# Kernel optimization log

Hardware: AMD Instinct MI355X
Metric: run time of the kernel (lower is better)

Reference implementation:

```python
import jax, jax.numpy as jnp
import numpy as np

NUM_LINKS = 1048576


def _euler_rots(theta):
    # theta: [N,3] -> per-link rotation R = Rz @ Ry @ Rx, shape [N,3,3]
    cx, cy, cz = jnp.cos(theta[:, 0]), jnp.cos(theta[:, 1]), jnp.cos(theta[:, 2])
    sx, sy, sz = jnp.sin(theta[:, 0]), jnp.sin(theta[:, 1]), jnp.sin(theta[:, 2])
    z = jnp.zeros_like(cx)
    o = jnp.ones_like(cx)
    rx = jnp.stack([jnp.stack([o, z, z], -1),
                    jnp.stack([z, cx, -sx], -1),
                    jnp.stack([z, sx, cx], -1)], -2)
    ry = jnp.stack([jnp.stack([cy, z, sy], -1),
                    jnp.stack([z, o, z], -1),
                    jnp.stack([-sy, z, cy], -1)], -2)
    rz = jnp.stack([jnp.stack([cz, -sz, z], -1),
                    jnp.stack([sz, cz, z], -1),
                    jnp.stack([z, z, o], -1)], -2)
    return jnp.matmul(rz, jnp.matmul(ry, rx))  # [N,3,3]


def setup_inputs() -> dict:
    key = jax.random.key(0)
    k1, k2 = jax.random.split(key)
    link_lengths = jax.random.uniform(k1, (NUM_LINKS,), dtype=jnp.float32)
    theta = jax.random.normal(k2, (NUM_LINKS, 3), dtype=jnp.float32)
    return {"link_lengths": link_lengths, "theta": theta}


def reference(link_lengths, theta):
    # Original loop computes eff_pos_i = sum_{j=0..i} (R_0 @ R_1 @ ... @ R_j) @ t_j
    # with t_j = l_j * e_z. Vectorize via prefix matrix products + cumsum.
    R = _euler_rots(theta)                                   # [N,3,3]
    P = jax.lax.associative_scan(jnp.matmul, R)              # P_j = R_0@...@R_j
    v = P[:, :, 2] * link_lengths[:, None]                   # P_j @ (l_j * e_z)
    return jnp.cumsum(v, axis=0)                             # [N,3]
```

## Files before the change

### kernel.cpp

```cpp
#include <hip/hip_runtime.h>
#include <math.h>


#define K1_TPB 512
#define K1_EPT 2
#define K1_EPB (K1_TPB * K1_EPT)
#define K1_NW (K1_TPB / 64)
#define K2_TPB 256
#define K2_EPT 4
#define K2_EPB (K2_TPB * K2_EPT)
#define MAXB 1024
#define EPG (MAXB / K2_TPB)

struct Xf {
    float m[9];
    float p[3];
};

__device__ __forceinline__ void xf_identity(Xf& x) {
    x.m[0] = 1.f; x.m[1] = 0.f; x.m[2] = 0.f;
    x.m[3] = 0.f; x.m[4] = 1.f; x.m[5] = 0.f;
    x.m[6] = 0.f; x.m[7] = 0.f; x.m[8] = 1.f;
    x.p[0] = 0.f; x.p[1] = 0.f; x.p[2] = 0.f;
}

__device__ __forceinline__ Xf xf_comb(const Xf& A, const Xf& B) {
    Xf o;
#pragma unroll
    for (int r = 0; r < 3; ++r) {
        const float a0 = A.m[r * 3 + 0], a1 = A.m[r * 3 + 1], a2 = A.m[r * 3 + 2];
#pragma unroll
        for (int c = 0; c < 3; ++c) {
            o.m[r * 3 + c] = a0 * B.m[0 * 3 + c] + a1 * B.m[1 * 3 + c] + a2 * B.m[2 * 3 + c];
        }
        o.p[r] = A.p[r] + a0 * B.p[0] + a1 * B.p[1] + a2 * B.p[2];
    }
    return o;
}

__device__ __forceinline__ void xf_fold(Xf& a, float ax, float ay, float az, float l) {
    float sx, cx, sy, cy, sz, cz;
    sincosf(ax, &sx, &cx);
    sincosf(ay, &sy, &cy);
    sincosf(az, &sz, &cz);
    const float sysx = sy * sx, sycx = sy * cx;
    const float r00 = cz * cy;
    const float r01 = cz * sysx - sz * cx;
    const float r02 = sz * sx + cz * sycx;
    const float r10 = sz * cy;
    const float r11 = cz * cx + sz * sysx;
    const float r12 = sz * sycx - cz * sx;
    const float r20 = -sy;
    const float r21 = cy * sx;
    const float r22 = cy * cx;
    const float t0 = l * r02, t1 = l * r12, t2 = l * r22;
    const float p0 = a.p[0] + a.m[0] * t0 + a.m[1] * t1 + a.m[2] * t2;
    const float p1 = a.p[1] + a.m[3] * t0 + a.m[4] * t1 + a.m[5] * t2;
    const float p2 = a.p[2] + a.m[6] * t0 + a.m[7] * t1 + a.m[8] * t2;
    const float n0 = a.m[0] * r00 + a.m[1] * r10 + a.m[2] * r20;
    const float n1 = a.m[0] * r01 + a.m[1] * r11 + a.m[2] * r21;
    const float n2 = a.m[0] * r02 + a.m[1] * r12 + a.m[2] * r22;
    const float n3 = a.m[3] * r00 + a.m[4] * r10 + a.m[5] * r20;
    const float n4 = a.m[3] * r01 + a.m[4] * r11 + a.m[5] * r21;
    const float n5 = a.m[3] * r02 + a.m[4] * r12 + a.m[5] * r22;
    const float n6 = a.m[6] * r00 + a.m[7] * r10 + a.m[8] * r20;
    const float n7 = a.m[6] * r01 + a.m[7] * r11 + a.m[8] * r21;
    const float n8 = a.m[6] * r02 + a.m[7] * r12 + a.m[8] * r22;
    a.m[0] = n0; a.m[1] = n1; a.m[2] = n2;
    a.m[3] = n3; a.m[4] = n4; a.m[5] = n5;
    a.m[6] = n6; a.m[7] = n7; a.m[8] = n8;
    a.p[0] = p0; a.p[1] = p1; a.p[2] = p2;
}

__device__ __forceinline__ Xf xf_shfl_up(const Xf& a, int delta) {
    Xf o;
#pragma unroll
    for (int k = 0; k < 9; ++k) o.m[k] = __shfl_up(a.m[k], delta, 64);
#pragma unroll
    for (int k = 0; k < 3; ++k) o.p[k] = __shfl_up(a.p[k], delta, 64);
    return o;
}
__device__ __forceinline__ Xf xf_shfl_down(const Xf& a, int delta) {
    Xf o;
#pragma unroll
    for (int k = 0; k < 9; ++k) o.m[k] = __shfl_down(a.m[k], delta, 64);
#pragma unroll
    for (int k = 0; k < 3; ++k) o.p[k] = __shfl_down(a.p[k], delta, 64);
    return o;
}

__device__ __forceinline__ Xf wave_scan(Xf a, int lane) {
#pragma unroll
    for (int off = 1; off < 64; off <<= 1) {
        const Xf b = xf_shfl_up(a, off);
        if (lane >= off) a = xf_comb(b, a);
    }
    return a;
}

__device__ __forceinline__ Xf wave_reduce(Xf v, int lane) {
#pragma unroll
    for (int off = 1; off < 64; off <<= 1) {
        const Xf b = xf_shfl_down(v, off);
        if (lane + off < 64) v = xf_comb(v, b);
    }
    return v;
}

__device__ __forceinline__ Xf xf_load4(const Xf* p) {
    const float4* g = (const float4*)p;
    const float4 x = g[0], y = g[1], z = g[2];
    Xf b;
    b.m[0] = x.x; b.m[1] = x.y; b.m[2] = x.z;
    b.m[3] = x.w; b.m[4] = y.x; b.m[5] = y.y;
    b.m[6] = y.z; b.m[7] = y.w; b.m[8] = z.x;
    b.p[0] = z.y; b.p[1] = z.z; b.p[2] = z.w;
    return b;
}
__device__ __forceinline__ void xf_store4(Xf* p, const Xf& b) {
    float4* g = (float4*)p;
    g[0] = make_float4(b.m[0], b.m[1], b.m[2], b.m[3]);
    g[1] = make_float4(b.m[4], b.m[5], b.m[6], b.m[7]);
    g[2] = make_float4(b.m[8], b.p[0], b.p[1], b.p[2]);
}

__device__ __forceinline__ void xf_apply(const Xf& T, float q0, float q1, float q2,
                                         float& o0, float& o1, float& o2) {
    o0 = T.p[0] + T.m[0] * q0 + T.m[1] * q1 + T.m[2] * q2;
    o1 = T.p[1] + T.m[3] * q0 + T.m[4] * q1 + T.m[5] * q2;
    o2 = T.p[2] + T.m[6] * q0 + T.m[7] * q1 + T.m[8] * q2;
}

__global__ void __launch_bounds__(K1_TPB, 6)
fk_local(const float* __restrict__ ll, const float* __restrict__ th,
         Xf* __restrict__ agg, float* __restrict__ out, int n) {
    __shared__ Xf wagg[K1_NW];
    const int t = threadIdx.x, bid = blockIdx.x;
    const int lane = t & 63, w = t >> 6;
    const long long j0 = (long long)bid * K1_EPB + (long long)t * K1_EPT;

    Xf a;
    xf_identity(a);
    float pe[K1_EPT][3];
    if (j0 + K1_EPT <= n) {
        const float2* th2 = (const float2*)(th + 3 * j0);
        const float2 d0 = th2[0], d1 = th2[1], d2 = th2[2];
        const float2 L = *(const float2*)(ll + j0);
        xf_fold(a, d0.x, d0.y, d1.x, L.x);
        pe[0][0] = a.p[0]; pe[0][1] = a.p[1]; pe[0][2] = a.p[2];
        xf_fold(a, d1.y, d2.x, d2.y, L.y);
        pe[1][0] = a.p[0]; pe[1][1] = a.p[1]; pe[1][2] = a.p[2];
    } else {
#pragma unroll
        for (int e = 0; e < K1_EPT; ++e) {
            const long long j = j0 + e;
            if (j < n) xf_fold(a, th[3 * j + 0], th[3 * j + 1], th[3 * j + 2], ll[j]);
            pe[e][0] = a.p[0]; pe[e][1] = a.p[1]; pe[e][2] = a.p[2];
        }
    }

    const Xf inc = wave_scan(a, lane);
    if (lane == 63) wagg[w] = inc;
    __syncthreads();

    Xf exw;
    xf_identity(exw);
    for (int k = 0; k < w; ++k) exw = xf_comb(exw, wagg[k]);

    if (t == K1_TPB - 1) xf_store4(&agg[bid], xf_comb(exw, inc));

    const Xf ext = xf_shfl_up(inc, 1);
    Xf T = exw;
    if (lane != 0) T = xf_comb(T, ext);

    if (j0 + K1_EPT <= n) {
        float o0, o1, o2, o3, o4, o5;
        xf_apply(T, pe[0][0], pe[0][1], pe[0][2], o0, o1, o2);
        xf_apply(T, pe[1][0], pe[1][1], pe[1][2], o3, o4, o5);
        float2* q2 = (float2*)(out + 3 * j0);
        q2[0] = make_float2(o0, o1);
        q2[1] = make_float2(o2, o3);
        q2[2] = make_float2(o4, o5);
    } else {
#pragma unroll
        for (int e = 0; e < K1_EPT; ++e) {
            const long long j = j0 + e;
            if (j < n) {
                float o0, o1, o2;
                xf_apply(T, pe[e][0], pe[e][1], pe[e][2], o0, o1, o2);
                out[3 * j + 0] = o0; out[3 * j + 1] = o1; out[3 * j + 2] = o2;
            }
        }
    }
}

__global__ void __launch_bounds__(K2_TPB)
fk_fixup(const Xf* __restrict__ agg, float* __restrict__ out, int n, int nb) {
    __shared__ Xf wred[K2_TPB / 64];
    __shared__ Xf shG;
    const int t = threadIdx.x, bid = blockIdx.x;
    const int lane = t & 63, w = t >> 6;

    {
        const int i0 = t * EPG;
        Xf A;
        xf_identity(A);
#pragma unroll
        for (int e = 0; e < EPG; ++e) {
            const int i = i0 + e;
            if (i < bid) A = xf_comb(A, xf_load4(&agg[i]));
        }
        const Xf red = wave_reduce(A, lane);
        if (lane == 0) wred[w] = red;
    }
    __syncthreads();
    if (t == 0) {
        Xf G = wred[0];
#pragma unroll
        for (int k = 1; k < K2_TPB / 64; ++k) G = xf_comb(G, wred[k]);
        shG = G;
    }
    __syncthreads();
    const Xf G = shG;

    const long long j0 = (long long)bid * K2_EPB + (long long)t * K2_EPT;
    if (j0 + K2_EPT <= n) {
        float4* o4 = (float4*)(out + 3 * j0);
        const float4 x = o4[0], y = o4[1], z = o4[2];
        float r[12];
        xf_apply(G, x.x, x.y, x.z, r[0], r[1], r[2]);
        xf_apply(G, x.w, y.x, y.y, r[3], r[4], r[5]);
        xf_apply(G, y.z, y.w, z.x, r[6], r[7], r[8]);
        xf_apply(G, z.y, z.z, z.w, r[9], r[10], r[11]);
        o4[0] = make_float4(r[0], r[1], r[2], r[3]);
        o4[1] = make_float4(r[4], r[5], r[6], r[7]);
        o4[2] = make_float4(r[8], r[9], r[10], r[11]);
    } else {
#pragma unroll
        for (int e = 0; e < K2_EPT; ++e) {
            const long long j = j0 + e;
            if (j < n) {
                float o0, o1, o2;
                xf_apply(G, out[3 * j + 0], out[3 * j + 1], out[3 * j + 2], o0, o1, o2);
                out[3 * j + 0] = o0; out[3 * j + 1] = o1; out[3 * j + 2] = o2;
            }
        }
    }
}

extern "C" void kernel_launch(void* const* d_in, const int* in_sizes, int n_in,
                              void* d_out, int out_size, void* d_ws, size_t ws_size,
                              hipStream_t stream) {
    const float* ll = (const float*)d_in[0];
    const float* th = (const float*)d_in[1];
    float* out = (float*)d_out;
    const int n = in_sizes[0];

    int nb = (n + K1_EPB - 1) / K1_EPB;
    if (nb > MAXB) nb = MAXB;

    Xf* agg = (Xf*)d_ws;

    fk_local<<<nb, K1_TPB, 0, stream>>>(ll, th, agg, out, n);
    fk_fixup<<<nb, K2_TPB, 0, stream>>>(agg, out, n, nb);
}
```

Measured before the change: 29.80 us.

## Use DPP wave scans, fast sincos, and a single-block aggregate prefix kernel

Result: slower. 36.16 us (+21.3%).

```diff
diff --git a/kernel.cpp b/kernel.cpp
--- a/kernel.cpp
+++ b/kernel.cpp
@@ -6,11 +6,11 @@
 #define K1_EPT 2
 #define K1_EPB (K1_TPB * K1_EPT)
 #define K1_NW (K1_TPB / 64)
-#define K2_TPB 256
-#define K2_EPT 4
-#define K2_EPB (K2_TPB * K2_EPT)
+#define K3_TPB 256
+#define K3_EPT 4
+#define K3_EPB (K3_TPB * K3_EPT)
 #define MAXB 1024
-#define EPG (MAXB / K2_TPB)
+#define EPG (MAXB / 256)
 
 struct Xf {
     float m[9];
@@ -38,11 +38,33 @@
     return o;
 }
 
+__device__ __forceinline__ void fast_sincos(float x, float& s, float& c) {
+    const float fn = __builtin_rintf(x * 0.636619772367581343f);
+    const int n = (int)fn;
+    float r = __builtin_fmaf(fn, -1.57079637050628662109375f, x);
+    r = __builtin_fmaf(fn, 4.37113900018624283e-8f, r);
+    const float r2 = r * r;
+    float sp = __builtin_fmaf(r2, -1.9515295891e-4f, 8.3321608736e-3f);
+    sp = __builtin_fmaf(r2, sp, -1.6666654611e-1f);
+    const float ss = __builtin_fmaf(r * r2, sp, r);
+    float cp = __builtin_fmaf(r2, 2.443315711809948e-5f, -1.388731625493765e-3f);
+    cp = __builtin_fmaf(r2, cp, 4.166664568298827e-2f);
+    const float cc = __builtin_fmaf(r2 * r2, cp,
+                                    __builtin_fmaf(r2, -0.5f, 1.0f));
+    const int q = n & 3;
+    const float s0 = (q & 1) ? cc : ss;
+    const float c0 = (q & 1) ? ss : cc;
+    const unsigned sgn_s = (unsigned)(q & 2) << 30;
+    const unsigned sgn_c = (unsigned)((q + 1) & 2) << 30;
+    s = __uint_as_float(__float_as_uint(s0) ^ sgn_s);
+    c = __uint_as_float(__float_as_uint(c0) ^ sgn_c);
+}
+
 __device__ __forceinline__ void xf_fold(Xf& a, float ax, float ay, float az, float l) {
     float sx, cx, sy, cy, sz, cz;
-    sincosf(ax, &sx, &cx);
-    sincosf(ay, &sy, &cy);
-    sincosf(az, &sz, &cz);
+    fast_sincos(ax, sx, cx);
+    fast_sincos(ay, sy, cy);
+    fast_sincos(az, sz, cz);
     const float sysx = sy * sx, sycx = sy * cx;
     const float r00 = cz * cy;
     const float r01 = cz * sysx - sz * cx;
@@ -72,39 +94,47 @@
     a.p[0] = p0; a.p[1] = p1; a.p[2] = p2;
 }
 
-__device__ __forceinline__ Xf xf_shfl_up(const Xf& a, int delta) {
+template <int CTRL, int RMASK>
+__device__ __forceinline__ float dpp_f(float src, float oldv) {
+    return __int_as_float(__builtin_amdgcn_update_dpp(
+        __float_as_int(oldv), __float_as_int(src), CTRL, RMASK, 0xF, false));
+}
+
+template <int CTRL, int RMASK>
+__device__ __forceinline__ Xf xf_scan_step(const Xf& v) {
+    Xf b;
+    b.m[0] = dpp_f<CTRL, RMASK>(v.m[0], 1.f);
+    b.m[1] = dpp_f<CTRL, RMASK>(v.m[1], 0.f);
+    b.m[2] = dpp_f<CTRL, RMASK>(v.m[2], 0.f);
+    b.m[3] = dpp_f<CTRL, RMASK>(v.m[3], 0.f);
+    b.m[4] = dpp_f<CTRL, RMASK>(v.m[4], 1.f);
+    b.m[5] = dpp_f<CTRL, RMASK>(v.m[5], 0.f);
+    b.m[6] = dpp_f<CTRL, RMASK>(v.m[6], 0.f);
+    b.m[7] = dpp_f<CTRL, RMASK>(v.m[7], 0.f);
+    b.m[8] = dpp_f<CTRL, RMASK>(v.m[8], 1.f);
+    b.p[0] = dpp_f<CTRL, RMASK>(v.p[0], 0.f);
+    b.p[1] = dpp_f<CTRL, RMASK>(v.p[1], 0.f);
+    b.p[2] = dpp_f<CTRL, RMASK>(v.p[2], 0.f);
+    return xf_comb(b, v);
+}
+
+__device__ __forceinline__ Xf wave_scan(Xf v) {
+    v = xf_scan_step<0x111, 0xF>(v);
+    v = xf_scan_step<0x112, 0xF>(v);
+    v = xf_scan_step<0x114, 0xF>(v);
+    v = xf_scan_step<0x118, 0xF>(v);
+    v = xf_scan_step<0x142, 0xA>(v);
+    v = xf_scan_step<0x143, 0xC>(v);
+    return v;
+}
+
+__device__ __forceinline__ Xf xf_shfl_up1(const Xf& a) {
     Xf o;
 #pragma unroll
-    for (int k = 0; k < 9; ++k) o.m[k] = __shfl_up(a.m[k], delta, 64);
-#pragma unroll
-    for (int k = 0; k < 3; ++k) o.p[k] = __shfl_up(a.p[k], delta, 64);
+    for (int k = 0; k < 9; ++k) o.m[k] = __shfl_up(a.m[k], 1, 64);
+#pragma unroll
+    for (int k = 0; k < 3; ++k) o.p[k] = __shfl_up(a.p[k], 1, 64);
     return o;
-}
-__device__ __forceinline__ Xf xf_shfl_down(const Xf& a, int delta) {
-    Xf o;
-#pragma unroll
-    for (int k = 0; k < 9; ++k) o.m[k] = __shfl_down(a.m[k], delta, 64);
-#pragma unroll
-    for (int k = 0; k < 3; ++k) o.p[k] = __shfl_down(a.p[k], delta, 64);
-    return o;
-}
-
-__device__ __forceinline__ Xf wave_scan(Xf a, int lane) {
-#pragma unroll
-    for (int off = 1; off < 64; off <<= 1) {
-        const Xf b = xf_shfl_up(a, off);
-        if (lane >= off) a = xf_comb(b, a);
-    }
-    return a;
-}
-
-__device__ __forceinline__ Xf wave_reduce(Xf v, int lane) {
-#pragma unroll
-    for (int off = 1; off < 64; off <<= 1) {
-        const Xf b = xf_shfl_down(v, off);
-        if (lane + off < 64) v = xf_comb(v, b);
-    }
-    return v;
 }
 
 __device__ __forceinline__ Xf xf_load4(const Xf* p) {
@@ -131,7 +161,7 @@
     o2 = T.p[2] + T.m[6] * q0 + T.m[7] * q1 + T.m[8] * q2;
 }
 
-__global__ void __launch_bounds__(K1_TPB, 6)
+__global__ void __launch_bounds__(K1_TPB, 8)
 fk_local(const float* __restrict__ ll, const float* __restrict__ th,
          Xf* __restrict__ agg, float* __restrict__ out, int n) {
     __shared__ Xf wagg[K1_NW];
@@ -159,7 +189,7 @@
         }
     }
 
-    const Xf inc = wave_scan(a, lane);
+    const Xf inc = wave_scan(a);
     if (lane == 63) wagg[w] = inc;
     __syncthreads();
 
@@ -169,7 +199,7 @@
 
     if (t == K1_TPB - 1) xf_store4(&agg[bid], xf_comb(exw, inc));
 
-    const Xf ext = xf_shfl_up(inc, 1);
+    const Xf ext = xf_shfl_up1(inc);
     Xf T = exw;
     if (lane != 0) T = xf_comb(T, ext);
 
@@ -194,37 +224,52 @@
     }
 }
 
-__global__ void __launch_bounds__(K2_TPB)
-fk_fixup(const Xf* __restrict__ agg, float* __restrict__ out, int n, int nb) {
-    __shared__ Xf wred[K2_TPB / 64];
-    __shared__ Xf shG;
+__global__ void __launch_bounds__(256)
+fk_scanagg(const Xf* __restrict__ agg, Xf* __restrict__ pfx, int nb) {
+    __shared__ Xf wagg[4];
+    const int t = threadIdx.x;
+    const int lane = t & 63, w = t >> 6;
+    const int i0 = t * EPG;
+
+    Xf q[EPG];
+    Xf a;
+    xf_identity(a);
+#pragma unroll
+    for (int e = 0; e < EPG; ++e) {
+        const int i = i0 + e;
+        if (i < nb) a = xf_comb(a, xf_load4(&agg[i]));
+        q[e] = a;
+    }
+
+    const Xf inc = wave_scan(a);
+    if (lane == 63) wagg[w] = inc;
+    __syncthreads();
+
+    Xf exw;
+    xf_identity(exw);
+    for (int k = 0; k < w; ++k) exw = xf_comb(exw, wagg[k]);
+
+    const Xf ext = xf_shfl_up1(inc);
+    Xf T = exw;
+    if (lane != 0) T = xf_comb(T, ext);
+
+    if (i0 < nb) xf_store4(&pfx[i0], T);
+#pragma unroll
+    for (int e = 1; e < EPG; ++e) {
+        if (i0 + e < nb) {
+            Xf v = xf_comb(T, q[e - 1]);
+            xf_store4(&pfx[i0 + e], v);
+        }
+    }
+}
+
+__global__ void __launch_bounds__(K3_TPB, 8)
+fk_fixup(const Xf* __restrict__ pfx, float* __restrict__ out, int n) {
     const int t = threadIdx.x, bid = blockIdx.x;
-    const int lane = t & 63, w = t >> 6;
-
-    {
-        const int i0 = t * EPG;
-        Xf A;
-        xf_identity(A);
-#pragma unroll
-        for (int e = 0; e < EPG; ++e) {
-            const int i = i0 + e;
-            if (i < bid) A = xf_comb(A, xf_load4(&agg[i]));
-        }
-        const Xf red = wave_reduce(A, lane);
-        if (lane == 0) wred[w] = red;
-    }
-    __syncthreads();
-    if (t == 0) {
-        Xf G = wred[0];
-#pragma unroll
-        for (int k = 1; k < K2_TPB / 64; ++k) G = xf_comb(G, wred[k]);
-        shG = G;
-    }
-    __syncthreads();
-    const Xf G = shG;
-
-    const long long j0 = (long long)bid * K2_EPB + (long long)t * K2_EPT;
-    if (j0 + K2_EPT <= n) {
+    const Xf G = xf_load4(&pfx[bid]);
+
+    const long long j0 = (long long)bid * K3_EPB + (long long)t * K3_EPT;
+    if (j0 + K3_EPT <= n) {
         float4* o4 = (float4*)(out + 3 * j0);
         const float4 x = o4[0], y = o4[1], z = o4[2];
         float r[12];
@@ -237,7 +282,7 @@
         o4[2] = make_float4(r[8], r[9], r[10], r[11]);
     } else {
 #pragma unroll
-        for (int e = 0; e < K2_EPT; ++e) {
+        for (int e = 0; e < K3_EPT; ++e) {
             const long long j = j0 + e;
             if (j < n) {
                 float o0, o1, o2;
@@ -260,7 +305,9 @@
     if (nb > MAXB) nb = MAXB;
 
     Xf* agg = (Xf*)d_ws;
+    Xf* pfx = agg + MAXB;
 
     fk_local<<<nb, K1_TPB, 0, stream>>>(ll, th, agg, out, n);
-    fk_fixup<<<nb, K2_TPB, 0, stream>>>(agg, out, n, nb);
-}
+    fk_scanagg<<<1, 256, 0, stream>>>(agg, pfx, nb);
+    fk_fixup<<<nb, K3_TPB, 0, stream>>>(pfx, out, n);
+}
```
